# Performance work log

Hardware: AMD Instinct MI355X
Metric: run time of the kernel (lower is better)

The kernel has to match this reference:

```python
import jax, jax.numpy as jnp
import numpy as np

N_HEAD = 12

def setup_inputs() -> dict:
    key = jax.random.key(0)
    k1, k2, k3 = jax.random.split(key, 3)
    B, T, C = 2, 4096, 768
    x = jax.random.normal(k1, (B, T, C), dtype=jnp.float32)
    Wqkv = jax.random.normal(k2, (C, 3 * C), dtype=jnp.float32) * (1.0 / np.sqrt(C))
    bqkv = jnp.zeros((3 * C,), dtype=jnp.float32)
    Wout = jax.random.normal(k3, (C, C), dtype=jnp.float32) * (1.0 / np.sqrt(C))
    bout = jnp.zeros((C,), dtype=jnp.float32)
    return {"x": x, "Wqkv": Wqkv, "bqkv": bqkv, "Wout": Wout, "bout": bout}

def reference(x, Wqkv, bqkv, Wout, bout):
    B, T, C = x.shape
    H = N_HEAD
    D = C // H
    qkv = x @ Wqkv + bqkv                       # [B,T,3C]
    qkv = qkv.reshape(B, T, 3, H, D)
    q = qkv[:, :, 0].transpose(0, 2, 1, 3)       # [B,H,T,D]
    k = qkv[:, :, 1].transpose(0, 2, 1, 3)
    v = qkv[:, :, 2].transpose(0, 2, 1, 3)
    att = jnp.einsum('bhqd,bhkd->bhqk', q, k) / jnp.sqrt(jnp.float32(D))
    causal = jnp.tril(jnp.ones((T, T), dtype=bool))
    att = jnp.where(causal[None, None], att, jnp.float32(-jnp.inf))
    att = jax.nn.softmax(att, axis=-1)
    out = jnp.einsum('bhqk,bhkd->bhqd', att, v)  # [B,H,T,D]
    out = out.transpose(0, 2, 1, 3).reshape(B, T, C)
    return out @ Wout + bout
```

## Files before the change

kernel.cpp:

```cpp
#include <hip/hip_runtime.h>
#include <math.h>

#define Bb 2
#define Tt 4096
#define Cc 768
#define Hh 12
#define Dd 64

typedef __attribute__((ext_vector_type(8))) short short8;
typedef __attribute__((ext_vector_type(4))) float f32x4;
typedef __attribute__((ext_vector_type(4))) unsigned short u16x4;

static __device__ __forceinline__ unsigned short f2bf(float f) {
    unsigned u = __float_as_uint(f);
    u += 0x7FFF + ((u >> 16) & 1);
    return (unsigned short)(u >> 16);
}

static __device__ __forceinline__ float ex2(float x) {
    return __builtin_amdgcn_exp2f(x);
}

static __device__ __forceinline__ void gload16(const void* g, void* l) {
    __builtin_amdgcn_global_load_lds(
        (const __attribute__((address_space(1))) unsigned*)g,
        (__attribute__((address_space(3))) unsigned*)l, 16, 0, 0);
}

__global__ __launch_bounds__(256)
void cvt_bf16(const float* __restrict__ in, unsigned short* __restrict__ out, int n8) {
    int i = blockIdx.x * 256 + threadIdx.x;
    if (i >= n8) return;
    float4 a = *(const float4*)(in + (size_t)i * 8);
    float4 b = *(const float4*)(in + (size_t)i * 8 + 4);
    union { short8 v; unsigned short u[8]; } p;
    p.u[0] = f2bf(a.x); p.u[1] = f2bf(a.y); p.u[2] = f2bf(a.z); p.u[3] = f2bf(a.w);
    p.u[4] = f2bf(b.x); p.u[5] = f2bf(b.y); p.u[6] = f2bf(b.z); p.u[7] = f2bf(b.w);
    *(short8*)(out + (size_t)i * 8) = p.v;
}

__global__ __launch_bounds__(256)
void transpose_w(const float* __restrict__ W, unsigned short* __restrict__ Wt,
                 int K, int N) {
    __shared__ __align__(16) unsigned short Tl[64][72];
    int n0 = blockIdx.x * 64, k0 = blockIdx.y * 64;
    int t = threadIdx.x;
    int r = t >> 2, c = (t & 3) * 16;
    const float* wp = W + (size_t)(k0 + r) * N + n0 + c;
    #pragma unroll
    for (int j = 0; j < 16; j += 4) {
        float4 v = *(const float4*)(wp + j);
        Tl[c + j + 0][r] = f2bf(v.x);
        Tl[c + j + 1][r] = f2bf(v.y);
        Tl[c + j + 2][r] = f2bf(v.z);
        Tl[c + j + 3][r] = f2bf(v.w);
    }
    __syncthreads();
    unsigned short* op = Wt + (size_t)(n0 + r) * K + k0 + c;
    *(short8*)op       = *(const short8*)&Tl[r][c];
    *(short8*)(op + 8) = *(const short8*)&Tl[r][c + 8];
}

template<bool BF16OUT>
__global__ __launch_bounds__(256)
void gemm_mfma(const unsigned short* __restrict__ A, const unsigned short* __restrict__ Bt,
               const float* __restrict__ bias, void* __restrict__ Cout,
               int M, int N, int K, int qcols,
               unsigned short* __restrict__ vtb, int voff) {
    union SmemU {
        unsigned short ab[2][128][64];
        unsigned short tv[128][136];
    };
    __shared__ __align__(16) SmemU sh;
    const int tid = threadIdx.x;
    const int wid = tid >> 6, lane = tid & 63;
    const int lr = lane & 15, g = lane >> 4;
    const int wr = wid >> 1, wc = wid & 1;
    const int m0 = blockIdx.y * 128, n0 = blockIdx.x * 128;
    const int srow = lane >> 3;
    const int scol = (lane & 7) * 8;

    f32x4 acc[4][4] = {};

    for (int k0 = 0; k0 < K; k0 += 64) {
        #pragma unroll
        for (int j = 0; j < 4; ++j) {
            int ci = wid * 4 + j;
            int row = ci * 8 + srow;
            gload16(A  + (size_t)(m0 + row) * K + k0 + scol, &sh.ab[0][ci * 8][0]);
            gload16(Bt + (size_t)(n0 + row) * K + k0 + scol, &sh.ab[1][ci * 8][0]);
        }
        __syncthreads();
        #pragma unroll
        for (int ks = 0; ks < 2; ++ks) {
            short8 af[4], bfr[4];
            #pragma unroll
            for (int m = 0; m < 4; ++m)
                af[m] = *(const short8*)&sh.ab[0][wr * 64 + m * 16 + lr][ks * 32 + g * 8];
            #pragma unroll
            for (int n = 0; n < 4; ++n)
                bfr[n] = *(const short8*)&sh.ab[1][wc * 64 + n * 16 + lr][ks * 32 + g * 8];
            #pragma unroll
            for (int m = 0; m < 4; ++m)
                #pragma unroll
                for (int n = 0; n < 4; ++n)
                    acc[m][n] = __builtin_amdgcn_mfma_f32_16x16x32_bf16(
                        af[m], bfr[n], acc[m][n], 0, 0, 0);
        }
        __syncthreads();
    }

    if (vtb != nullptr && n0 >= voff) {
        #pragma unroll
        for (int n = 0; n < 4; ++n) {
            int tcol = wc * 64 + n * 16 + lr;
            float bv = bias[n0 + tcol];
            #pragma unroll
            for (int m = 0; m < 4; ++m) {
                int trow = wr * 64 + m * 16 + g * 4;
                #pragma unroll
                for (int r = 0; r < 4; ++r)
                    sh.tv[tcol][trow + r] = f2bf(acc[m][n][r] + bv);
            }
        }
        __syncthreads();
        const int dlocal = tid >> 1;
        const int th     = (tid & 1) * 64;
        const int colg   = n0 + dlocal;
        const int hd     = (colg - voff) >> 6;
        const int d      = (colg - voff) & 63;
        const int token  = m0 + th;
        const int bq     = token >> 12;
        const int t0     = token & (Tt - 1);
        unsigned short* dst = vtb + ((size_t)(bq * Hh + hd) * Dd + d) * Tt + t0;
        const unsigned short* src = &sh.tv[dlocal][th];
        #pragma unroll
        for (int j = 0; j < 8; ++j)
            *(short8*)(dst + j * 8) = *(const short8*)(src + j * 8);
        return;
    }

    const float qscale = 0.125f * 1.44269504088896340736f;
    #pragma unroll
    for (int n = 0; n < 4; ++n) {
        int coln = n0 + wc * 64 + n * 16 + lr;
        float bv = bias[coln];
        float sc = (coln < qcols) ? qscale : 1.0f;
        #pragma unroll
        for (int m = 0; m < 4; ++m) {
            int rowb = m0 + wr * 64 + m * 16 + g * 4;
            #pragma unroll
            for (int r = 0; r < 4; ++r) {
                float v = (acc[m][n][r] + bv) * sc;
                if (BF16OUT)
                    ((unsigned short*)Cout)[(size_t)(rowb + r) * N + coln] = f2bf(v);
                else
                    ((float*)Cout)[(size_t)(rowb + r) * N + coln] = v;
            }
        }
    }
}

__global__ __launch_bounds__(256)
void attn_mfma(const unsigned short* __restrict__ qkvb,
               const unsigned short* __restrict__ vtb,
               unsigned short* __restrict__ outb) {
    const int nid  = blockIdx.x;
    const int xcd  = nid & 7;
    const int rest = nid >> 3;
    const int P    = rest & 31;
    const int H2   = xcd + 8 * (rest >> 5);
    const int hd   = H2 % Hh;
    const int b    = H2 / Hh;
    const int tid = threadIdx.x;
    const int wid = tid >> 6, lane = tid & 63;
    const int lr = lane & 15, g = lane >> 4;
    const int rm7 = lr & 7;
    const size_t rs = 3 * Cc;

    __shared__ __align__(16) unsigned short Ks[2][64 * 64];
    __shared__ __align__(16) unsigned short Vs[2][64 * 64];

    const unsigned short* qkvbase = qkvb + (size_t)b * Tt * rs;
    const unsigned short* vbase   = vtb + (size_t)((b * Hh + hd) * Dd) * Tt;

    const int srw  = lane >> 3;
    const int row0 = wid * 8 + srw;
    const int slog = (lane & 7) ^ (srw & 7);
    const unsigned short* ksrc0 = qkvbase + (size_t)row0 * rs + Cc + hd * Dd + slog * 8;
    const unsigned short* vsrc0 = vbase + (size_t)row0 * Tt + slog * 8;

    const int ntA = 64 - P;
    const int ntB = P + 1;

    auto stage = [&](int buf, int t) {
        gload16(ksrc0 + (size_t)t * 64 * rs,        &Ks[buf][wid * 512]);
        gload16(ksrc0 + (size_t)(t * 64 + 32) * rs, &Ks[buf][2048 + wid * 512]);
        gload16(vsrc0 + t * 64,                     &Vs[buf][wid * 512]);
        gload16(vsrc0 + (size_t)32 * Tt + t * 64,   &Vs[buf][2048 + wid * 512]);
    };

    stage(0, 0);
    __syncthreads();
    int cur = 0;

    const int laneA = lr + ((g & 1) << 5);
    const int laneB = laneA + 16;
    const int asel  = g >> 1;

    #pragma unroll 1
    for (int pass = 0; pass < 2; ++pass) {
        const int q0  = (pass ? P : 63 - P) * 64;
        const int nt  = pass ? ntB : ntA;
        const int myq = q0 + wid * 16 + lr;

        short8 qf0, qf1;
        {
            const unsigned short* qp = qkvbase + (size_t)myq * rs + hd * Dd;
            qf0 = *(const short8*)(qp + g * 8);
            qf1 = *(const short8*)(qp + 32 + g * 8);
        }

        f32x4 o[4];
        #pragma unroll
        for (int dt = 0; dt < 4; ++dt) o[dt] = (f32x4){0.f, 0.f, 0.f, 0.f};
        float lpart = 0.f;

        #pragma unroll 1
        for (int kbt = 0; kbt < nt; ++kbt) {
            if (kbt + 1 < nt)       stage(cur ^ 1, kbt + 1);
            else if (pass == 0)     stage(cur ^ 1, 0);

            const unsigned short* Kc = &Ks[cur][0];
            const unsigned short* Vc = &Vs[cur][0];

            f32x4 st[4];
            __builtin_amdgcn_s_setprio(1);
            #pragma unroll
            for (int kt = 0; kt < 4; ++kt) {
                int row = kt * 16 + lr;
                int off0 = row * 64 + (g ^ rm7) * 8;
                short8 kf0 = *(const short8*)&Kc[off0];
                short8 kf1 = *(const short8*)&Kc[off0 ^ 32];
                f32x4 a = (f32x4){0.f, 0.f, 0.f, 0.f};
                a = __builtin_amdgcn_mfma_f32_16x16x32_bf16(kf0, qf0, a, 0, 0, 0);
                a = __builtin_amdgcn_mfma_f32_16x16x32_bf16(kf1, qf1, a, 0, 0, 0);
                st[kt] = a;
            }
            __builtin_amdgcn_s_setprio(0);

            if (kbt == nt - 1) {
                #pragma unroll
                for (int kt = 0; kt < 4; ++kt)
                    #pragma unroll
                    for (int r = 0; r < 4; ++r)
                        if (kbt * 64 + kt * 16 + g * 4 + r > myq) st[kt][r] = -1e30f;
            }

            float psum = 0.f;
            #pragma unroll
            for (int kt = 0; kt < 4; ++kt)
                #pragma unroll
                for (int r = 0; r < 4; ++r) {
                    float p = ex2(st[kt][r]);
                    st[kt][r] = p;
                    psum += p;
                }
            lpart += psum;

            unsigned up[4][2];
            #pragma unroll
            for (int kt = 0; kt < 4; ++kt) {
                asm("v_cvt_pk_bf16_f32 %0, %1, %2"
                    : "=v"(up[kt][0]) : "v"(st[kt][0]), "v"(st[kt][1]));
                asm("v_cvt_pk_bf16_f32 %0, %1, %2"
                    : "=v"(up[kt][1]) : "v"(st[kt][2]), "v"(st[kt][3]));
            }
            #pragma unroll
            for (int ks = 0; ks < 2; ++ks) {
                unsigned wa0 = __shfl(up[2 * ks][0],     laneA);
                unsigned wb0 = __shfl(up[2 * ks + 1][0], laneA);
                unsigned wa1 = __shfl(up[2 * ks][1],     laneA);
                unsigned wb1 = __shfl(up[2 * ks + 1][1], laneA);
                unsigned wa2 = __shfl(up[2 * ks][0],     laneB);
                unsigned wb2 = __shfl(up[2 * ks + 1][0], laneB);
                unsigned wa3 = __shfl(up[2 * ks][1],     laneB);
                unsigned wb3 = __shfl(up[2 * ks + 1][1], laneB);
                union { unsigned w[4]; short8 v; } pb;
                pb.w[0] = asel ? wb0 : wa0;
                pb.w[1] = asel ? wb1 : wa1;
                pb.w[2] = asel ? wb2 : wa2;
                pb.w[3] = asel ? wb3 : wa3;
                __builtin_amdgcn_s_setprio(1);
                #pragma unroll
                for (int dt = 0; dt < 4; ++dt) {
                    int row = dt * 16 + lr;
                    int off = row * 64 + (((ks << 2) | g) ^ rm7) * 8;
                    short8 vf = *(const short8*)&Vc[off];
                    o[dt] = __builtin_amdgcn_mfma_f32_16x16x32_bf16(vf, pb.v, o[dt], 0, 0, 0);
                }
                __builtin_amdgcn_s_setprio(0);
            }

            __syncthreads();
            cur ^= 1;
        }

        float l_r = lpart;
        l_r += __shfl_xor(l_r, 16);
        l_r += __shfl_xor(l_r, 32);

        float inv = 1.f / fmaxf(l_r, 1e-37f);
        unsigned short* op = outb + ((size_t)b * Tt + myq) * Cc + hd * Dd + g * 4;
        #pragma unroll
        for (int dt = 0; dt < 4; ++dt) {
            u16x4 w;
            #pragma unroll
            for (int r = 0; r < 4; ++r) w[r] = f2bf(o[dt][r] * inv);
            *(u16x4*)(op + dt * 16) = w;
        }
    }
}

extern "C" void kernel_launch(void* const* d_in, const int* in_sizes, int n_in,
                              void* d_out, int out_size, void* d_ws, size_t ws_size,
                              hipStream_t stream) {
    const float* x    = (const float*)d_in[0];
    const float* Wqkv = (const float*)d_in[1];
    const float* bqkv = (const float*)d_in[2];
    const float* Wout = (const float*)d_in[3];
    const float* bout = (const float*)d_in[4];
    float* out = (float*)d_out;

    const int M = Bb * Tt;
    const int N1 = 3 * Cc;

    char* p = (char*)d_ws;
    unsigned short* qkvb  = (unsigned short*)p; p += (size_t)M * N1 * 2;
    unsigned short* xb    = (unsigned short*)p; p += (size_t)M * Cc * 2;
    unsigned short* wqkvt = (unsigned short*)p; p += (size_t)N1 * Cc * 2;
    unsigned short* woutt = (unsigned short*)p; p += (size_t)Cc * Cc * 2;
    unsigned short* vtb   = (unsigned short*)p; p += (size_t)Bb * Hh * Dd * Tt * 2;
    unsigned short* attb  = (unsigned short*)p; p += (size_t)M * Cc * 2;

    cvt_bf16<<<dim3((M * Cc / 8 + 255) / 256), dim3(256), 0, stream>>>(x, xb, M * Cc / 8);
    transpose_w<<<dim3(N1 / 64, Cc / 64), dim3(256), 0, stream>>>(Wqkv, wqkvt, Cc, N1);
    transpose_w<<<dim3(Cc / 64, Cc / 64), dim3(256), 0, stream>>>(Wout, woutt, Cc, Cc);

    gemm_mfma<true><<<dim3(N1 / 128, M / 128), dim3(256), 0, stream>>>(
        xb, wqkvt, bqkv, qkvb, M, N1, Cc, Cc, vtb, 2 * Cc);

    attn_mfma<<<dim3(32 * Hh * Bb), dim3(256), 0, stream>>>(qkvb, vtb, attb);

    gemm_mfma<false><<<dim3(Cc / 128, M / 128), dim3(256), 0, stream>>>(
        attb, woutt, bout, out, M, Cc, Cc, 0, nullptr, 1 << 30);
}
```

Baseline: 201.4 us.

## Triple-buffer K/V tiles and merge both causal passes into one flat loop

Replaces the two-pass double-buffered attention loop with a single flattened loop over all 65 key tiles. K/V shared-memory staging moves to three buffers, with a two-tile prefetch distance and explicit vmcnt waits plus a single barrier per iteration. Both query fragments are preloaded up front, and the pass switch happens mid-loop through an inline epilogue. This aims to hide global-load latency and remove the pipeline drain between passes, at the cost of 50% more LDS per block, which may lower occupancy.

```diff
diff --git a/kernel.cpp b/kernel.cpp
--- a/kernel.cpp
+++ b/kernel.cpp
@@ -178,8 +178,8 @@
     const int rm7 = lr & 7;
     const size_t rs = 3 * Cc;
 
-    __shared__ __align__(16) unsigned short Ks[2][64 * 64];
-    __shared__ __align__(16) unsigned short Vs[2][64 * 64];
+    __shared__ __align__(16) unsigned short Ks[3][64 * 64];
+    __shared__ __align__(16) unsigned short Vs[3][64 * 64];
 
     const unsigned short* qkvbase = qkvb + (size_t)b * Tt * rs;
     const unsigned short* vbase   = vtb + (size_t)((b * Hh + hd) * Dd) * Tt;
@@ -191,9 +191,21 @@
     const unsigned short* vsrc0 = vbase + (size_t)row0 * Tt + slog * 8;
 
     const int ntA = 64 - P;
-    const int ntB = P + 1;
-
-    auto stage = [&](int buf, int t) {
+    const int qA  = (63 - P) * 64 + wid * 16 + lr;
+    const int qB  = P * 64 + wid * 16 + lr;
+
+    short8 qfA0, qfA1, qfB0, qfB1;
+    {
+        const unsigned short* qp = qkvbase + (size_t)qA * rs + hd * Dd;
+        qfA0 = *(const short8*)(qp + g * 8);
+        qfA1 = *(const short8*)(qp + 32 + g * 8);
+        qp = qkvbase + (size_t)qB * rs + hd * Dd;
+        qfB0 = *(const short8*)(qp + g * 8);
+        qfB1 = *(const short8*)(qp + 32 + g * 8);
+    }
+
+    auto stage = [&](int buf, int ts) {
+        int t = (ts < ntA) ? ts : ts - ntA;
         gload16(ksrc0 + (size_t)t * 64 * rs,        &Ks[buf][wid * 512]);
         gload16(ksrc0 + (size_t)(t * 64 + 32) * rs, &Ks[buf][2048 + wid * 512]);
         gload16(vsrc0 + t * 64,                     &Vs[buf][wid * 512]);
@@ -201,115 +213,23 @@
     };
 
     stage(0, 0);
-    __syncthreads();
-    int cur = 0;
+    stage(1, 1);
 
     const int laneA = lr + ((g & 1) << 5);
     const int laneB = laneA + 16;
     const int asel  = g >> 1;
 
-    #pragma unroll 1
-    for (int pass = 0; pass < 2; ++pass) {
-        const int q0  = (pass ? P : 63 - P) * 64;
-        const int nt  = pass ? ntB : ntA;
-        const int myq = q0 + wid * 16 + lr;
-
-        short8 qf0, qf1;
-        {
-            const unsigned short* qp = qkvbase + (size_t)myq * rs + hd * Dd;
-            qf0 = *(const short8*)(qp + g * 8);
-            qf1 = *(const short8*)(qp + 32 + g * 8);
-        }
-
-        f32x4 o[4];
-        #pragma unroll
-        for (int dt = 0; dt < 4; ++dt) o[dt] = (f32x4){0.f, 0.f, 0.f, 0.f};
-        float lpart = 0.f;
-
-        #pragma unroll 1
-        for (int kbt = 0; kbt < nt; ++kbt) {
-            if (kbt + 1 < nt)       stage(cur ^ 1, kbt + 1);
-            else if (pass == 0)     stage(cur ^ 1, 0);
-
-            const unsigned short* Kc = &Ks[cur][0];
-            const unsigned short* Vc = &Vs[cur][0];
-
-            f32x4 st[4];
-            __builtin_amdgcn_s_setprio(1);
-            #pragma unroll
-            for (int kt = 0; kt < 4; ++kt) {
-                int row = kt * 16 + lr;
-                int off0 = row * 64 + (g ^ rm7) * 8;
-                short8 kf0 = *(const short8*)&Kc[off0];
-                short8 kf1 = *(const short8*)&Kc[off0 ^ 32];
-                f32x4 a = (f32x4){0.f, 0.f, 0.f, 0.f};
-                a = __builtin_amdgcn_mfma_f32_16x16x32_bf16(kf0, qf0, a, 0, 0, 0);
-                a = __builtin_amdgcn_mfma_f32_16x16x32_bf16(kf1, qf1, a, 0, 0, 0);
-                st[kt] = a;
-            }
-            __builtin_amdgcn_s_setprio(0);
-
-            if (kbt == nt - 1) {
-                #pragma unroll
-                for (int kt = 0; kt < 4; ++kt)
-                    #pragma unroll
-                    for (int r = 0; r < 4; ++r)
-                        if (kbt * 64 + kt * 16 + g * 4 + r > myq) st[kt][r] = -1e30f;
-            }
-
-            float psum = 0.f;
-            #pragma unroll
-            for (int kt = 0; kt < 4; ++kt)
-                #pragma unroll
-                for (int r = 0; r < 4; ++r) {
-                    float p = ex2(st[kt][r]);
-                    st[kt][r] = p;
-                    psum += p;
-                }
-            lpart += psum;
-
-            unsigned up[4][2];
-            #pragma unroll
-            for (int kt = 0; kt < 4; ++kt) {
-                asm("v_cvt_pk_bf16_f32 %0, %1, %2"
-                    : "=v"(up[kt][0]) : "v"(st[kt][0]), "v"(st[kt][1]));
-                asm("v_cvt_pk_bf16_f32 %0, %1, %2"
-                    : "=v"(up[kt][1]) : "v"(st[kt][2]), "v"(st[kt][3]));
-            }
-            #pragma unroll
-            for (int ks = 0; ks < 2; ++ks) {
-                unsigned wa0 = __shfl(up[2 * ks][0],     laneA);
-                unsigned wb0 = __shfl(up[2 * ks + 1][0], laneA);
-                unsigned wa1 = __shfl(up[2 * ks][1],     laneA);
-                unsigned wb1 = __shfl(up[2 * ks + 1][1], laneA);
-                unsigned wa2 = __shfl(up[2 * ks][0],     laneB);
-                unsigned wb2 = __shfl(up[2 * ks + 1][0], laneB);
-                unsigned wa3 = __shfl(up[2 * ks][1],     laneB);
-                unsigned wb3 = __shfl(up[2 * ks + 1][1], laneB);
-                union { unsigned w[4]; short8 v; } pb;
-                pb.w[0] = asel ? wb0 : wa0;
-                pb.w[1] = asel ? wb1 : wa1;
-                pb.w[2] = asel ? wb2 : wa2;
-                pb.w[3] = asel ? wb3 : wa3;
-                __builtin_amdgcn_s_setprio(1);
-                #pragma unroll
-                for (int dt = 0; dt < 4; ++dt) {
-                    int row = dt * 16 + lr;
-                    int off = row * 64 + (((ks << 2) | g) ^ rm7) * 8;
-                    short8 vf = *(const short8*)&Vc[off];
-                    o[dt] = __builtin_amdgcn_mfma_f32_16x16x32_bf16(vf, pb.v, o[dt], 0, 0, 0);
-                }
-                __builtin_amdgcn_s_setprio(0);
-            }
-
-            __syncthreads();
-            cur ^= 1;
-        }
-
+    f32x4 o[4];
+    #pragma unroll
+    for (int dt = 0; dt < 4; ++dt) o[dt] = (f32x4){0.f, 0.f, 0.f, 0.f};
+    float lpart = 0.f;
+    short8 qf0 = qfA0, qf1 = qfA1;
+    int myq = qA;
+
+    auto epilogue = [&]() {
         float l_r = lpart;
         l_r += __shfl_xor(l_r, 16);
         l_r += __shfl_xor(l_r, 32);
-
         float inv = 1.f / fmaxf(l_r, 1e-37f);
         unsigned short* op = outb + ((size_t)b * Tt + myq) * Cc + hd * Dd + g * 4;
         #pragma unroll
@@ -319,7 +239,101 @@
             for (int r = 0; r < 4; ++r) w[r] = f2bf(o[dt][r] * inv);
             *(u16x4*)(op + dt * 16) = w;
         }
-    }
+    };
+
+    #pragma unroll 1
+    for (int ts = 0; ts < 65; ++ts) {
+        if (ts < 64) asm volatile("s_waitcnt vmcnt(4)" ::: "memory");
+        else         asm volatile("s_waitcnt vmcnt(0)" ::: "memory");
+        __builtin_amdgcn_s_barrier();
+        __builtin_amdgcn_sched_barrier(0);
+        if (ts + 2 < 65) stage((ts + 2) % 3, ts + 2);
+
+        const int inA = (ts < ntA) ? 1 : 0;
+        const int kbt = inA ? ts : ts - ntA;
+        const int nt  = inA ? ntA : (65 - ntA);
+        const unsigned short* Kc = &Ks[ts % 3][0];
+        const unsigned short* Vc = &Vs[ts % 3][0];
+
+        f32x4 st[4];
+        __builtin_amdgcn_s_setprio(1);
+        #pragma unroll
+        for (int kt = 0; kt < 4; ++kt) {
+            int row = kt * 16 + lr;
+            int off0 = row * 64 + (g ^ rm7) * 8;
+            short8 kf0 = *(const short8*)&Kc[off0];
+            short8 kf1 = *(const short8*)&Kc[off0 ^ 32];
+            f32x4 a = (f32x4){0.f, 0.f, 0.f, 0.f};
+            a = __builtin_amdgcn_mfma_f32_16x16x32_bf16(kf0, qf0, a, 0, 0, 0);
+            a = __builtin_amdgcn_mfma_f32_16x16x32_bf16(kf1, qf1, a, 0, 0, 0);
+            st[kt] = a;
+        }
+        __builtin_amdgcn_s_setprio(0);
+
+        if (kbt == nt - 1) {
+            #pragma unroll
+            for (int kt = 0; kt < 4; ++kt)
+                #pragma unroll
+                for (int r = 0; r < 4; ++r)
+                    if (kbt * 64 + kt * 16 + g * 4 + r > myq) st[kt][r] = -1e30f;
+        }
+
+        float psum = 0.f;
+        #pragma unroll
+        for (int kt = 0; kt < 4; ++kt)
+            #pragma unroll
+            for (int r = 0; r < 4; ++r) {
+                float p = ex2(st[kt][r]);
+                st[kt][r] = p;
+                psum += p;
+            }
+        lpart += psum;
+
+        unsigned up[4][2];
+        #pragma unroll
+        for (int kt = 0; kt < 4; ++kt) {
+            asm("v_cvt_pk_bf16_f32 %0, %1, %2"
+                : "=v"(up[kt][0]) : "v"(st[kt][0]), "v"(st[kt][1]));
+            asm("v_cvt_pk_bf16_f32 %0, %1, %2"
+                : "=v"(up[kt][1]) : "v"(st[kt][2]), "v"(st[kt][3]));
+        }
+        #pragma unroll
+        for (int ks = 0; ks < 2; ++ks) {
+            unsigned wa0 = __shfl(up[2 * ks][0],     laneA);
+            unsigned wb0 = __shfl(up[2 * ks + 1][0], laneA);
+            unsigned wa1 = __shfl(up[2 * ks][1],     laneA);
+            unsigned wb1 = __shfl(up[2 * ks + 1][1], laneA);
+            unsigned wa2 = __shfl(up[2 * ks][0],     laneB);
+            unsigned wb2 = __shfl(up[2 * ks + 1][0], laneB);
+            unsigned wa3 = __shfl(up[2 * ks][1],     laneB);
+            unsigned wb3 = __shfl(up[2 * ks + 1][1], laneB);
+            union { unsigned w[4]; short8 v; } pb;
+            pb.w[0] = asel ? wb0 : wa0;
+            pb.w[1] = asel ? wb1 : wa1;
+            pb.w[2] = asel ? wb2 : wa2;
+            pb.w[3] = asel ? wb3 : wa3;
+            __builtin_amdgcn_s_setprio(1);
+            #pragma unroll
+            for (int dt = 0; dt < 4; ++dt) {
+                int row = dt * 16 + lr;
+                int off = row * 64 + (((ks << 2) | g) ^ rm7) * 8;
+                short8 vf = *(const short8*)&Vc[off];
+                o[dt] = __builtin_amdgcn_mfma_f32_16x16x32_bf16(vf, pb.v, o[dt], 0, 0, 0);
+            }
+            __builtin_amdgcn_s_setprio(0);
+        }
+
+        if (ts == ntA - 1) {
+            epilogue();
+            #pragma unroll
+            for (int dt = 0; dt < 4; ++dt) o[dt] = (f32x4){0.f, 0.f, 0.f, 0.f};
+            lpart = 0.f;
+            qf0 = qfB0; qf1 = qfB1;
+            myq = qB;
+        }
+    }
+
+    epilogue();
 }
 
 extern "C" void kernel_launch(void* const* d_in, const int* in_sizes, int n_in,
```

After: 201.3 us. Within noise of the previous version (-0.0%).
